# Performance work log

Hardware: AMD Instinct MI355X
Metric: run time of the kernel (lower is better)

Reference implementation:

```python
import math
import jax, jax.numpy as jnp
import numpy as np

B, N, D, H = 2, 2048, 1024, 16

def setup_inputs() -> dict:
    key = jax.random.key(0)
    ks = jax.random.split(key, 5)
    x = jax.random.normal(ks[0], (B, N, D), dtype=jnp.float32)
    # causal mask: True = masked (matches masked_fill semantics)
    mask = jnp.broadcast_to(jnp.triu(jnp.ones((N, N), dtype=bool), k=1), (B, N, N))
    sc = 0.02
    Wqkv = jax.random.normal(ks[1], (3 * D, D), dtype=jnp.float32) * sc
    bqkv = jax.random.normal(ks[2], (3 * D,), dtype=jnp.float32) * sc
    Wo = jax.random.normal(ks[3], (D, D), dtype=jnp.float32) * sc
    bo = jax.random.normal(ks[4], (D,), dtype=jnp.float32) * sc
    return {"x": x, "mask": mask, "Wqkv": Wqkv, "bqkv": bqkv, "Wo": Wo, "bo": bo}

def reference(x, mask, Wqkv, bqkv, Wo, bo):
    b, n, d = x.shape
    h = H
    s = d // h
    qkv = x @ Wqkv.T + bqkv                       # [b, n, 3d]
    q, k, v = jnp.split(qkv, 3, axis=2)           # each [b, n, d]
    def heads(z):
        return z.reshape(b, n, h, s).transpose(0, 2, 1, 3)  # [b, h, n, s]
    q, k, v = heads(q), heads(k), heads(v)
    q = q / jnp.asarray(math.sqrt(s), q.dtype)
    a = jnp.einsum('bhqs,bhks->bhqk', q, k)       # [b, h, n, n]
    a = jnp.where(mask[:, None, :, :], -jnp.inf, a)
    a = jax.nn.softmax(a, axis=-1)
    y = jnp.einsum('bhqk,bhks->bhqs', a, v)       # [b, h, n, s]
    y = y.transpose(0, 2, 1, 3).reshape(b, n, d)
    return y @ Wo.T + bo
```

## Files before the change

### kernel.cpp

```cpp
#include <hip/hip_runtime.h>
#include <hip/hip_bf16.h>
#include <stdint.h>

#define BB 2
#define NN 2048
#define DD 1024
#define HH 16
#define SS 64

typedef short short8 __attribute__((ext_vector_type(8)));
typedef float f32x4 __attribute__((ext_vector_type(4)));

__device__ __forceinline__ float bf2f(uint16_t u) {
    return __uint_as_float(((uint32_t)u) << 16);
}
__device__ __forceinline__ uint16_t f2bf(float f) {
    uint32_t u = __float_as_uint(f);
    return (uint16_t)((u + 0x7FFFu + ((u >> 16) & 1u)) >> 16);
}
__device__ __forceinline__ short8 cvt8(float4 a, float4 b) {
    short8 s;
    s[0] = (short)f2bf(a.x); s[1] = (short)f2bf(a.y);
    s[2] = (short)f2bf(a.z); s[3] = (short)f2bf(a.w);
    s[4] = (short)f2bf(b.x); s[5] = (short)f2bf(b.y);
    s[6] = (short)f2bf(b.z); s[7] = (short)f2bf(b.w);
    return s;
}

__device__ __forceinline__ void load_lds16(const uint16_t* g, uint16_t* l) {
    __builtin_amdgcn_global_load_lds(
        (const __attribute__((address_space(1))) void*)g,
        (__attribute__((address_space(3))) void*)l, 16, 0, 0);
}

#define XE  (4096 * 1024)
#define WQE (3072 * 1024)
#define WOE (1024 * 1024)

__global__ __launch_bounds__(256) void cvt_all(
    const float* __restrict__ x, const float* __restrict__ wq,
    const float* __restrict__ wo, uint16_t* __restrict__ dst)
{
    int i = (blockIdx.x * 256 + threadIdx.x) * 8;
    const float* src;
    int off;
    if (i < XE)            { src = x;  off = i; }
    else if (i < XE + WQE) { src = wq; off = i - XE; }
    else                   { src = wo; off = i - XE - WQE; }
    float4 a = *(const float4*)(src + off);
    float4 b = *(const float4*)(src + off + 4);
    *(short8*)(dst + i) = cvt8(a, b);
}

__global__ __launch_bounds__(256) void gemm_qkv(
    const uint16_t* __restrict__ X, const uint16_t* __restrict__ W,
    const float* __restrict__ bias,
    uint16_t* __restrict__ Qb, uint16_t* __restrict__ Kb, uint16_t* __restrict__ Vt)
{
    __shared__ __align__(16) uint16_t smem[18432];
    uint16_t* As0 = smem;
    uint16_t* As1 = smem + 4096;
    uint16_t* Bs0 = smem + 8192;
    uint16_t* Bs1 = smem + 12288;

    const int tid = threadIdx.x;
    const int w = tid >> 6, l = tid & 63;
    const int lq = l & 15, lg = l >> 4;
    const int wm = w >> 1, wn = w & 1;

    const int flat = blockIdx.x + blockIdx.y * 24;
    const int xcd = flat & 7, g = flat >> 3;
    const int n0 = (xcd * 3 + (g % 3)) * 128;
    const int m0 = (g / 3) * 128;

    f32x4 acc[4][4] = {};

    for (int k0 = 0; k0 < 1024; k0 += 64) {
        __syncthreads();
        #pragma unroll
        for (int j = 0; j < 2; ++j) {
            const int c = (j * 4 + w) * 64 + l;
            const size_t ra = (size_t)(m0 + (c >> 2)) * 1024 + k0 + (c & 3) * 8;
            const size_t rb = (size_t)(n0 + (c >> 2)) * 1024 + k0 + (c & 3) * 8;
            load_lds16(X + ra,      As0 + (j * 4 + w) * 512);
            load_lds16(X + ra + 32, As1 + (j * 4 + w) * 512);
            load_lds16(W + rb,      Bs0 + (j * 4 + w) * 512);
            load_lds16(W + rb + 32, Bs1 + (j * 4 + w) * 512);
        }
        __syncthreads();
        short8 af[4], bfr[4];
        #pragma unroll
        for (int mi = 0; mi < 4; ++mi)
            af[mi] = *(const short8*)&As0[(wm * 64 + mi * 16 + lq) * 32 + lg * 8];
        #pragma unroll
        for (int ni = 0; ni < 4; ++ni)
            bfr[ni] = *(const short8*)&Bs0[(wn * 64 + ni * 16 + lq) * 32 + lg * 8];
        #pragma unroll
        for (int mi = 0; mi < 4; ++mi)
            #pragma unroll
            for (int ni = 0; ni < 4; ++ni)
                acc[mi][ni] = __builtin_amdgcn_mfma_f32_16x16x32_bf16(
                    af[mi], bfr[ni], acc[mi][ni], 0, 0, 0);
        #pragma unroll
        for (int mi = 0; mi < 4; ++mi)
            af[mi] = *(const short8*)&As1[(wm * 64 + mi * 16 + lq) * 32 + lg * 8];
        #pragma unroll
        for (int ni = 0; ni < 4; ++ni)
            bfr[ni] = *(const short8*)&Bs1[(wn * 64 + ni * 16 + lq) * 32 + lg * 8];
        #pragma unroll
        for (int mi = 0; mi < 4; ++mi)
            #pragma unroll
            for (int ni = 0; ni < 4; ++ni)
                acc[mi][ni] = __builtin_amdgcn_mfma_f32_16x16x32_bf16(
                    af[mi], bfr[ni], acc[mi][ni], 0, 0, 0);
    }

    __syncthreads();
    const int part = n0 >> 10;
    const int hh = ((n0 + wn * 64) & 1023) >> 6;
    const int mrow0 = m0 + wm * 64;
    const int bh = (mrow0 >> 11) * 16 + hh;
    const int tok0 = mrow0 & 2047;
    const float scl = (part == 0) ? 0.125f * 1.44269504089f : 1.0f;

    float bias4[4];
    #pragma unroll
    for (int ni = 0; ni < 4; ++ni)
        bias4[ni] = bias[n0 + wn * 64 + ni * 16 + lq];

    uint16_t* T = smem + w * 4608;
    if (part < 2) {
        #pragma unroll
        for (int mi = 0; mi < 4; ++mi)
            #pragma unroll
            for (int ni = 0; ni < 4; ++ni)
                #pragma unroll
                for (int r = 0; r < 4; ++r)
                    T[(mi * 16 + lg * 4 + r) * 72 + ni * 16 + lq] =
                        f2bf((acc[mi][ni][r] + bias4[ni]) * scl);
    } else {
        #pragma unroll
        for (int mi = 0; mi < 4; ++mi)
            #pragma unroll
            for (int ni = 0; ni < 4; ++ni)
                #pragma unroll
                for (int r = 0; r < 4; ++r)
                    T[(ni * 16 + lq) * 72 + mi * 16 + lg * 4 + r] =
                        f2bf(acc[mi][ni][r] + bias4[ni]);
    }

    const int a0 = l >> 3, b8 = (l & 7) * 8;
    #pragma unroll
    for (int i = 0; i < 8; ++i) {
        int a = i * 8 + a0;
        short8 u = *(short8*)&T[a * 72 + b8];
        uint16_t* p;
        if (part < 2) {
            uint16_t* dst = (part == 0) ? Qb : Kb;
            p = dst + ((size_t)bh * 2048 + tok0 + a) * 64 + b8;
        } else {
            p = Vt + ((size_t)bh * 64 + a) * 2048 + tok0 + b8;
        }
        *(short8*)p = u;
    }
}

__device__ __forceinline__ void loadKf(const uint16_t* Kb, int kv0, int lq, int lg,
                                       short8 (&d)[8]) {
    #pragma unroll
    for (int n = 0; n < 4; ++n) {
        const uint16_t* kb = Kb + (size_t)(kv0 + n * 16 + lq) * 64 + lg * 8;
        d[2 * n]     = *(const short8*)kb;
        d[2 * n + 1] = *(const short8*)(kb + 32);
    }
}
__device__ __forceinline__ void loadVf(const uint16_t* Vb, int kv0, int lq, int lg,
                                       short8 (&d)[8]) {
    #pragma unroll
    for (int n = 0; n < 4; ++n) {
        const uint16_t* vb = Vb + (size_t)(n * 16 + lq) * 2048 + kv0 + lg * 8;
        d[2 * n]     = *(const short8*)vb;
        d[2 * n + 1] = *(const short8*)(vb + 32);
    }
}

#define DEFER_THR 11.5f

__global__ __launch_bounds__(128) void attn_mfma(
    const uint16_t* __restrict__ Q, const uint16_t* __restrict__ K,
    const uint16_t* __restrict__ Vt, uint16_t* __restrict__ Y)
{
    const int id = blockIdx.x;
    const int bh = id & 31;
    const int blk = 63 - (id >> 5);
    const int qt = blk >> 1;
    const int q0 = blk * 32;

    const int wv = threadIdx.x >> 6;
    const int lane = threadIdx.x & 63;
    const int lq = lane & 15;
    const int lg = lane >> 4;

    __shared__ __align__(16) uint16_t Pl[2][2][16][72];
    __shared__ float  My[32][68];
    __shared__ float2 Mml[32];

    const uint16_t* Kb = K + (size_t)bh * (2048 * 64);
    const uint16_t* Vb = Vt + (size_t)bh * (64 * 2048);
    const int b = bh >> 4, h = bh & 15;

    short8 qf[2][2];
    #pragma unroll
    for (int sub = 0; sub < 2; ++sub) {
        const uint16_t* qb = Q + ((size_t)bh * 2048 + q0 + sub * 16 + lq) * 64 + lg * 8;
        qf[sub][0] = *(const short8*)qb;
        qf[sub][1] = *(const short8*)(qb + 32);
    }

    f32x4 y[2][4] = {};
    float m[2]    = {-INFINITY, -INFINITY};
    float lsum[2] = {0.f, 0.f};

    short8 kf[8], vv[8];
    loadKf(Kb, wv * 64, lq, lg, kf);

    auto step = [&](int kv0, bool domask, bool pref) {
        loadVf(Vb, kv0, lq, lg, vv);

        f32x4 z[2][4];
        __builtin_amdgcn_s_setprio(1);
        #pragma unroll
        for (int sub = 0; sub < 2; ++sub)
            #pragma unroll
            for (int n = 0; n < 4; ++n) {
                f32x4 t = {};
                t = __builtin_amdgcn_mfma_f32_16x16x32_bf16(kf[2 * n], qf[sub][0], t, 0, 0, 0);
                z[sub][n] = __builtin_amdgcn_mfma_f32_16x16x32_bf16(kf[2 * n + 1], qf[sub][1], t, 0, 0, 0);
            }
        __builtin_amdgcn_s_setprio(0);

        if (pref) loadKf(Kb, kv0 + 128, lq, lg, kf);

        if (domask) {
            #pragma unroll
            for (int sub = 0; sub < 2; ++sub) {
                const int qrow = q0 + sub * 16 + lq;
                #pragma unroll
                for (int n = 0; n < 4; ++n) {
                    const int kvb = kv0 + n * 16 + lg * 4;
                    #pragma unroll
                    for (int r = 0; r < 4; ++r)
                        if (kvb + r > qrow) z[sub][n][r] = -INFINITY;
                }
            }
        }

        float mt[2];
        #pragma unroll
        for (int sub = 0; sub < 2; ++sub) {
            float t = -INFINITY;
            #pragma unroll
            for (int n = 0; n < 4; ++n)
                #pragma unroll
                for (int r = 0; r < 4; ++r)
                    t = fmaxf(t, z[sub][n][r]);
            mt[sub] = t;
        }
        const float g = fmaxf(mt[0] - m[0], mt[1] - m[1]);
        const bool skip = __all(g <= DEFER_THR);

        if (!skip) {
            #pragma unroll
            for (int sub = 0; sub < 2; ++sub) {
                float mf = fmaxf(mt[sub], __shfl_xor(mt[sub], 16));
                mf = fmaxf(mf, __shfl_xor(mf, 32));
                const float mn = fmaxf(m[sub], mf);
                const float sc = exp2f(m[sub] - mn);
                m[sub] = mn;
                lsum[sub] *= sc;
                float scy[4];
                #pragma unroll
                for (int r = 0; r < 4; ++r) scy[r] = __shfl(sc, lg * 4 + r);
                #pragma unroll
                for (int n = 0; n < 4; ++n)
                    #pragma unroll
                    for (int r = 0; r < 4; ++r)
                        y[sub][n][r] *= scy[r];
            }
        }

        float ps[2] = {0.f, 0.f};
        #pragma unroll
        for (int sub = 0; sub < 2; ++sub) {
            #pragma unroll
            for (int n = 0; n < 4; ++n) {
                float e0 = exp2f(z[sub][n][0] - m[sub]);
                float e1 = exp2f(z[sub][n][1] - m[sub]);
                float e2 = exp2f(z[sub][n][2] - m[sub]);
                float e3 = exp2f(z[sub][n][3] - m[sub]);
                ps[sub] += (e0 + e1) + (e2 + e3);
                uint32_t p0, p1;
                asm("v_cvt_pk_bf16_f32 %0, %1, %2" : "=v"(p0) : "v"(e0), "v"(e1));
                asm("v_cvt_pk_bf16_f32 %0, %1, %2" : "=v"(p1) : "v"(e2), "v"(e3));
                uint2 u; u.x = p0; u.y = p1;
                *(uint2*)&Pl[wv][sub][lq][n * 16 + lg * 4] = u;
            }
        }
        lsum[0] += ps[0];
        lsum[1] += ps[1];

        short8 pa[2][2];
        #pragma unroll
        for (int sub = 0; sub < 2; ++sub) {
            pa[sub][0] = *(short8*)&Pl[wv][sub][lq][lg * 8];
            pa[sub][1] = *(short8*)&Pl[wv][sub][lq][lg * 8 + 32];
        }

        __builtin_amdgcn_s_setprio(1);
        #pragma unroll
        for (int sub = 0; sub < 2; ++sub)
            #pragma unroll
            for (int n = 0; n < 4; ++n) {
                y[sub][n] = __builtin_amdgcn_mfma_f32_16x16x32_bf16(pa[sub][0], vv[2 * n], y[sub][n], 0, 0, 0);
                y[sub][n] = __builtin_amdgcn_mfma_f32_16x16x32_bf16(pa[sub][1], vv[2 * n + 1], y[sub][n], 0, 0, 0);
            }
        __builtin_amdgcn_s_setprio(0);
    };

    if (wv <= qt) {
        int kt = wv;
        for (; kt + 2 <= qt; kt += 2)
            step(kt * 64, false, true);
        step(kt * 64, kt == qt, false);
    }

    float ls[2];
    #pragma unroll
    for (int sub = 0; sub < 2; ++sub) {
        float t = lsum[sub];
        t += __shfl_xor(t, 16);
        t += __shfl_xor(t, 32);
        ls[sub] = t;
    }

    if (wv == 1) {
        #pragma unroll
        for (int sub = 0; sub < 2; ++sub) {
            #pragma unroll
            for (int n = 0; n < 4; ++n)
                #pragma unroll
                for (int r = 0; r < 4; ++r)
                    My[sub * 16 + lg * 4 + r][n * 16 + lq] = y[sub][n][r];
            if (lg == 0) Mml[sub * 16 + lq] = make_float2(m[sub], ls[sub]);
        }
    }
    __syncthreads();
    if (wv == 0) {
        #pragma unroll
        for (int sub = 0; sub < 2; ++sub) {
            float2 o = Mml[sub * 16 + lq];
            const float m1 = o.x, l1 = o.y;
            const float mx = fmaxf(m[sub], m1);
            const float w0 = exp2f(m[sub] - mx);
            const float w1 = exp2f(m1 - mx);
            const float inv = 1.0f / (ls[sub] * w0 + l1 * w1);
            const float f0 = w0 * inv, f1 = w1 * inv;
            float f0r[4], f1r[4];
            #pragma unroll
            for (int r = 0; r < 4; ++r) {
                f0r[r] = __shfl(f0, lg * 4 + r);
                f1r[r] = __shfl(f1, lg * 4 + r);
            }
            #pragma unroll
            for (int r = 0; r < 4; ++r) {
                int token = b * 2048 + q0 + sub * 16 + lg * 4 + r;
                uint16_t* yrow = Y + (size_t)token * 1024 + h * 64;
                #pragma unroll
                for (int n = 0; n < 4; ++n) {
                    float val = y[sub][n][r] * f0r[r] +
                                My[sub * 16 + lg * 4 + r][n * 16 + lq] * f1r[r];
                    yrow[n * 16 + lq] = f2bf(val);
                }
            }
        }
    }
}

__global__ __launch_bounds__(256) void gemm_proj(
    const uint16_t* __restrict__ Yin, const uint16_t* __restrict__ W,
    const float* __restrict__ bias, float* __restrict__ out)
{
    __shared__ __align__(16) uint16_t smem[16384];
    uint16_t* As0 = smem;
    uint16_t* As1 = smem + 4096;
    uint16_t* Bs0 = smem + 8192;
    uint16_t* Bs1 = smem + 12288;

    const int tid = threadIdx.x;
    const int w = tid >> 6, l = tid & 63;
    const int lq = l & 15, lg = l >> 4;
    const int wm = w >> 1, wn = w & 1;

    const int flat = blockIdx.x + blockIdx.y * 8;
    const int n0 = (flat & 7) * 128;
    const int m0 = (flat >> 3) * 128;

    f32x4 acc[4][4] = {};

    for (int k0 = 0; k0 < 1024; k0 += 64) {
        __syncthreads();
        #pragma unroll
        for (int j = 0; j < 2; ++j) {
            const int c = (j * 4 + w) * 64 + l;
            const size_t ra = (size_t)(m0 + (c >> 2)) * 1024 + k0 + (c & 3) * 8;
            const size_t rb = (size_t)(n0 + (c >> 2)) * 1024 + k0 + (c & 3) * 8;
            load_lds16(Yin + ra,      As0 + (j * 4 + w) * 512);
            load_lds16(Yin + ra + 32, As1 + (j * 4 + w) * 512);
            load_lds16(W + rb,        Bs0 + (j * 4 + w) * 512);
            load_lds16(W + rb + 32,   Bs1 + (j * 4 + w) * 512);
        }
        __syncthreads();
        short8 af[4], bfr[4];
        #pragma unroll
        for (int mi = 0; mi < 4; ++mi)
            af[mi] = *(const short8*)&As0[(wm * 64 + mi * 16 + lq) * 32 + lg * 8];
        #pragma unroll
        for (int ni = 0; ni < 4; ++ni)
            bfr[ni] = *(const short8*)&Bs0[(wn * 64 + ni * 16 + lq) * 32 + lg * 8];
        #pragma unroll
        for (int mi = 0; mi < 4; ++mi)
            #pragma unroll
            for (int ni = 0; ni < 4; ++ni)
                acc[mi][ni] = __builtin_amdgcn_mfma_f32_16x16x32_bf16(
                    af[mi], bfr[ni], acc[mi][ni], 0, 0, 0);
        #pragma unroll
        for (int mi = 0; mi < 4; ++mi)
            af[mi] = *(const short8*)&As1[(wm * 64 + mi * 16 + lq) * 32 + lg * 8];
        #pragma unroll
        for (int ni = 0; ni < 4; ++ni)
            bfr[ni] = *(const short8*)&Bs1[(wn * 64 + ni * 16 + lq) * 32 + lg * 8];
        #pragma unroll
        for (int mi = 0; mi < 4; ++mi)
            #pragma unroll
            for (int ni = 0; ni < 4; ++ni)
                acc[mi][ni] = __builtin_amdgcn_mfma_f32_16x16x32_bf16(
                    af[mi], bfr[ni], acc[mi][ni], 0, 0, 0);
    }

    const int mrow0 = m0 + wm * 64;
    const int ncol0 = n0 + wn * 64;
    float bias4[4];
    #pragma unroll
    for (int ni = 0; ni < 4; ++ni)
        bias4[ni] = bias[ncol0 + ni * 16 + lq];

    #pragma unroll
    for (int mi = 0; mi < 4; ++mi)
        #pragma unroll
        for (int r = 0; r < 4; ++r) {
            const size_t rowoff = (size_t)(mrow0 + mi * 16 + lg * 4 + r) * 1024;
            #pragma unroll
            for (int ni = 0; ni < 4; ++ni)
                out[rowoff + ncol0 + ni * 16 + lq] = acc[mi][ni][r] + bias4[ni];
        }
}


extern "C" void kernel_launch(void* const* d_in, const int* in_sizes, int n_in,
                              void* d_out, int out_size, void* d_ws, size_t ws_size,
                              hipStream_t stream) {
    const float* x    = (const float*)d_in[0];
    const float* Wqkv = (const float*)d_in[2];
    const float* bqkv = (const float*)d_in[3];
    const float* Wo   = (const float*)d_in[4];
    const float* bo   = (const float*)d_in[5];

    const size_t QK = (size_t)BB * HH * NN * SS;

    uint16_t* Xb  = (uint16_t*)d_ws;
    uint16_t* Wqb = Xb + XE;
    uint16_t* Wob = Wqb + WQE;
    uint16_t* Qb  = Wob + WOE;
    uint16_t* Kb  = Qb + QK;
    uint16_t* Vt  = Kb + QK;
    uint16_t* Yb  = Vt + QK;

    cvt_all<<<(XE + WQE + WOE) / 8 / 256, 256, 0, stream>>>(x, Wqkv, Wo, Xb);
    gemm_qkv<<<dim3(24, 32), 256, 0, stream>>>(Xb, Wqb, bqkv, Qb, Kb, Vt);
    attn_mfma<<<2048, 128, 0, stream>>>(Qb, Kb, Vt, Yb);
    gemm_proj<<<dim3(8, 32), 256, 0, stream>>>(Yb, Wob, bo, (float*)d_out);
}
```

Baseline: 139.6 us.

## Pair short and long causal query blocks per workgroup for load balance

The attention kernel now launches half as many workgroups. Each workgroup processes two query blocks, a short one (xp) and its mirrored long one (63-xp), so every workgroup does roughly the same causal work. K/V addressing also switches to precomputed per-lane pointers that advance by a fixed stride, which removes per-iteration index math. The cost is less parallelism (1024 blocks of 2 waves) and an extra __syncthreads per half, and the two halves run serially inside a block.

```diff
diff --git a/kernel.cpp b/kernel.cpp
--- a/kernel.cpp
+++ b/kernel.cpp
@@ -165,22 +165,18 @@
     }
 }
 
-__device__ __forceinline__ void loadKf(const uint16_t* Kb, int kv0, int lq, int lg,
-                                       short8 (&d)[8]) {
+__device__ __forceinline__ void loadK8(const uint16_t* kp, short8 (&d)[8]) {
     #pragma unroll
     for (int n = 0; n < 4; ++n) {
-        const uint16_t* kb = Kb + (size_t)(kv0 + n * 16 + lq) * 64 + lg * 8;
-        d[2 * n]     = *(const short8*)kb;
-        d[2 * n + 1] = *(const short8*)(kb + 32);
-    }
-}
-__device__ __forceinline__ void loadVf(const uint16_t* Vb, int kv0, int lq, int lg,
-                                       short8 (&d)[8]) {
+        d[2 * n]     = *(const short8*)(kp + n * 1024);
+        d[2 * n + 1] = *(const short8*)(kp + n * 1024 + 32);
+    }
+}
+__device__ __forceinline__ void loadV8(const uint16_t* vp, short8 (&d)[8]) {
     #pragma unroll
     for (int n = 0; n < 4; ++n) {
-        const uint16_t* vb = Vb + (size_t)(n * 16 + lq) * 2048 + kv0 + lg * 8;
-        d[2 * n]     = *(const short8*)vb;
-        d[2 * n + 1] = *(const short8*)(vb + 32);
+        d[2 * n]     = *(const short8*)(vp + n * 32768);
+        d[2 * n + 1] = *(const short8*)(vp + n * 32768 + 32);
     }
 }
 
@@ -192,9 +188,7 @@
 {
     const int id = blockIdx.x;
     const int bh = id & 31;
-    const int blk = 63 - (id >> 5);
-    const int qt = blk >> 1;
-    const int q0 = blk * 32;
+    const int xp = id >> 5;
 
     const int wv = threadIdx.x >> 6;
     const int lane = threadIdx.x & 63;
@@ -209,180 +203,194 @@
     const uint16_t* Vb = Vt + (size_t)bh * (64 * 2048);
     const int b = bh >> 4, h = bh & 15;
 
-    short8 qf[2][2];
-    #pragma unroll
-    for (int sub = 0; sub < 2; ++sub) {
-        const uint16_t* qb = Q + ((size_t)bh * 2048 + q0 + sub * 16 + lq) * 64 + lg * 8;
-        qf[sub][0] = *(const short8*)qb;
-        qf[sub][1] = *(const short8*)(qb + 32);
-    }
-
-    f32x4 y[2][4] = {};
-    float m[2]    = {-INFINITY, -INFINITY};
-    float lsum[2] = {0.f, 0.f};
-
-    short8 kf[8], vv[8];
-    loadKf(Kb, wv * 64, lq, lg, kf);
-
-    auto step = [&](int kv0, bool domask, bool pref) {
-        loadVf(Vb, kv0, lq, lg, vv);
-
-        f32x4 z[2][4];
-        __builtin_amdgcn_s_setprio(1);
-        #pragma unroll
-        for (int sub = 0; sub < 2; ++sub)
-            #pragma unroll
-            for (int n = 0; n < 4; ++n) {
-                f32x4 t = {};
-                t = __builtin_amdgcn_mfma_f32_16x16x32_bf16(kf[2 * n], qf[sub][0], t, 0, 0, 0);
-                z[sub][n] = __builtin_amdgcn_mfma_f32_16x16x32_bf16(kf[2 * n + 1], qf[sub][1], t, 0, 0, 0);
-            }
-        __builtin_amdgcn_s_setprio(0);
-
-        if (pref) loadKf(Kb, kv0 + 128, lq, lg, kf);
-
-        if (domask) {
+    for (int half = 0; half < 2; ++half) {
+        const int blk = half ? (63 - xp) : xp;
+        const int qt = blk >> 1;
+        const int q0 = blk * 32;
+
+        short8 qf[2][2];
+        #pragma unroll
+        for (int sub = 0; sub < 2; ++sub) {
+            const uint16_t* qb = Q + ((size_t)bh * 2048 + q0 + sub * 16 + lq) * 64 + lg * 8;
+            qf[sub][0] = *(const short8*)qb;
+            qf[sub][1] = *(const short8*)(qb + 32);
+        }
+
+        f32x4 y[2][4] = {};
+        float m[2]    = {-INFINITY, -INFINITY};
+        float lsum[2] = {0.f, 0.f};
+
+        const uint16_t* kp = Kb + ((size_t)(wv * 64 + lq)) * 64 + lg * 8;
+        const uint16_t* vp = Vb + (size_t)lq * 2048 + wv * 64 + lg * 8;
+
+        short8 kf[8], vv[8];
+        loadK8(kp, kf);
+
+        auto step = [&](int kv0, const uint16_t* vcur, const uint16_t* knext,
+                        bool domask, bool pref) {
+            loadV8(vcur, vv);
+
+            f32x4 z[2][4];
+            __builtin_amdgcn_s_setprio(1);
+            #pragma unroll
+            for (int sub = 0; sub < 2; ++sub)
+                #pragma unroll
+                for (int n = 0; n < 4; ++n) {
+                    f32x4 t = {};
+                    t = __builtin_amdgcn_mfma_f32_16x16x32_bf16(kf[2 * n], qf[sub][0], t, 0, 0, 0);
+                    z[sub][n] = __builtin_amdgcn_mfma_f32_16x16x32_bf16(kf[2 * n + 1], qf[sub][1], t, 0, 0, 0);
+                }
+            __builtin_amdgcn_s_setprio(0);
+
+            if (pref) loadK8(knext, kf);
+
+            if (domask) {
+                #pragma unroll
+                for (int sub = 0; sub < 2; ++sub) {
+                    const int qrow = q0 + sub * 16 + lq;
+                    #pragma unroll
+                    for (int n = 0; n < 4; ++n) {
+                        const int kvb = kv0 + n * 16 + lg * 4;
+                        #pragma unroll
+                        for (int r = 0; r < 4; ++r)
+                            if (kvb + r > qrow) z[sub][n][r] = -INFINITY;
+                    }
+                }
+            }
+
+            float mt[2];
             #pragma unroll
             for (int sub = 0; sub < 2; ++sub) {
-                const int qrow = q0 + sub * 16 + lq;
-                #pragma unroll
-                for (int n = 0; n < 4; ++n) {
-                    const int kvb = kv0 + n * 16 + lg * 4;
-                    #pragma unroll
-                    for (int r = 0; r < 4; ++r)
-                        if (kvb + r > qrow) z[sub][n][r] = -INFINITY;
-                }
-            }
-        }
-
-        float mt[2];
-        #pragma unroll
-        for (int sub = 0; sub < 2; ++sub) {
-            float t = -INFINITY;
-            #pragma unroll
-            for (int n = 0; n < 4; ++n)
-                #pragma unroll
-                for (int r = 0; r < 4; ++r)
-                    t = fmaxf(t, z[sub][n][r]);
-            mt[sub] = t;
-        }
-        const float g = fmaxf(mt[0] - m[0], mt[1] - m[1]);
-        const bool skip = __all(g <= DEFER_THR);
-
-        if (!skip) {
-            #pragma unroll
-            for (int sub = 0; sub < 2; ++sub) {
-                float mf = fmaxf(mt[sub], __shfl_xor(mt[sub], 16));
-                mf = fmaxf(mf, __shfl_xor(mf, 32));
-                const float mn = fmaxf(m[sub], mf);
-                const float sc = exp2f(m[sub] - mn);
-                m[sub] = mn;
-                lsum[sub] *= sc;
-                float scy[4];
-                #pragma unroll
-                for (int r = 0; r < 4; ++r) scy[r] = __shfl(sc, lg * 4 + r);
+                float t = -INFINITY;
                 #pragma unroll
                 for (int n = 0; n < 4; ++n)
                     #pragma unroll
                     for (int r = 0; r < 4; ++r)
-                        y[sub][n][r] *= scy[r];
-            }
-        }
-
-        float ps[2] = {0.f, 0.f};
+                        t = fmaxf(t, z[sub][n][r]);
+                mt[sub] = t;
+            }
+            const float g = fmaxf(mt[0] - m[0], mt[1] - m[1]);
+            const bool skip = __all(g <= DEFER_THR);
+
+            if (!skip) {
+                #pragma unroll
+                for (int sub = 0; sub < 2; ++sub) {
+                    float mf = fmaxf(mt[sub], __shfl_xor(mt[sub], 16));
+                    mf = fmaxf(mf, __shfl_xor(mf, 32));
+                    const float mn = fmaxf(m[sub], mf);
+                    const float sc = exp2f(m[sub] - mn);
+                    m[sub] = mn;
+                    lsum[sub] *= sc;
+                    float scy[4];
+                    #pragma unroll
+                    for (int r = 0; r < 4; ++r) scy[r] = __shfl(sc, lg * 4 + r);
+                    #pragma unroll
+                    for (int n = 0; n < 4; ++n)
+                        #pragma unroll
+                        for (int r = 0; r < 4; ++r)
+                            y[sub][n][r] *= scy[r];
+                }
+            }
+
+            float ps[2] = {0.f, 0.f};
+            #pragma unroll
+            for (int sub = 0; sub < 2; ++sub) {
+                #pragma unroll
+                for (int n = 0; n < 4; ++n) {
+                    float e0 = exp2f(z[sub][n][0] - m[sub]);
+                    float e1 = exp2f(z[sub][n][1] - m[sub]);
+                    float e2 = exp2f(z[sub][n][2] - m[sub]);
+                    float e3 = exp2f(z[sub][n][3] - m[sub]);
+                    ps[sub] += (e0 + e1) + (e2 + e3);
+                    uint32_t p0, p1;
+                    asm("v_cvt_pk_bf16_f32 %0, %1, %2" : "=v"(p0) : "v"(e0), "v"(e1));
+                    asm("v_cvt_pk_bf16_f32 %0, %1, %2" : "=v"(p1) : "v"(e2), "v"(e3));
+                    uint2 u; u.x = p0; u.y = p1;
+                    *(uint2*)&Pl[wv][sub][lq][n * 16 + lg * 4] = u;
+                }
+            }
+            lsum[0] += ps[0];
+            lsum[1] += ps[1];
+
+            short8 pa[2][2];
+            #pragma unroll
+            for (int sub = 0; sub < 2; ++sub) {
+                pa[sub][0] = *(short8*)&Pl[wv][sub][lq][lg * 8];
+                pa[sub][1] = *(short8*)&Pl[wv][sub][lq][lg * 8 + 32];
+            }
+
+            __builtin_amdgcn_s_setprio(1);
+            #pragma unroll
+            for (int sub = 0; sub < 2; ++sub)
+                #pragma unroll
+                for (int n = 0; n < 4; ++n) {
+                    y[sub][n] = __builtin_amdgcn_mfma_f32_16x16x32_bf16(pa[sub][0], vv[2 * n], y[sub][n], 0, 0, 0);
+                    y[sub][n] = __builtin_amdgcn_mfma_f32_16x16x32_bf16(pa[sub][1], vv[2 * n + 1], y[sub][n], 0, 0, 0);
+                }
+            __builtin_amdgcn_s_setprio(0);
+        };
+
+        if (wv <= qt) {
+            int kt = wv;
+            for (; kt + 2 <= qt; kt += 2) {
+                step(kt * 64, vp, kp + 8192, false, true);
+                kp += 8192;
+                vp += 128;
+            }
+            step(kt * 64, vp, kp, kt == qt, false);
+        }
+
+        float ls[2];
         #pragma unroll
         for (int sub = 0; sub < 2; ++sub) {
-            #pragma unroll
-            for (int n = 0; n < 4; ++n) {
-                float e0 = exp2f(z[sub][n][0] - m[sub]);
-                float e1 = exp2f(z[sub][n][1] - m[sub]);
-                float e2 = exp2f(z[sub][n][2] - m[sub]);
-                float e3 = exp2f(z[sub][n][3] - m[sub]);
-                ps[sub] += (e0 + e1) + (e2 + e3);
-                uint32_t p0, p1;
-                asm("v_cvt_pk_bf16_f32 %0, %1, %2" : "=v"(p0) : "v"(e0), "v"(e1));
-                asm("v_cvt_pk_bf16_f32 %0, %1, %2" : "=v"(p1) : "v"(e2), "v"(e3));
-                uint2 u; u.x = p0; u.y = p1;
-                *(uint2*)&Pl[wv][sub][lq][n * 16 + lg * 4] = u;
-            }
-        }
-        lsum[0] += ps[0];
-        lsum[1] += ps[1];
-
-        short8 pa[2][2];
-        #pragma unroll
-        for (int sub = 0; sub < 2; ++sub) {
-            pa[sub][0] = *(short8*)&Pl[wv][sub][lq][lg * 8];
-            pa[sub][1] = *(short8*)&Pl[wv][sub][lq][lg * 8 + 32];
-        }
-
-        __builtin_amdgcn_s_setprio(1);
-        #pragma unroll
-        for (int sub = 0; sub < 2; ++sub)
-            #pragma unroll
-            for (int n = 0; n < 4; ++n) {
-                y[sub][n] = __builtin_amdgcn_mfma_f32_16x16x32_bf16(pa[sub][0], vv[2 * n], y[sub][n], 0, 0, 0);
-                y[sub][n] = __builtin_amdgcn_mfma_f32_16x16x32_bf16(pa[sub][1], vv[2 * n + 1], y[sub][n], 0, 0, 0);
-            }
-        __builtin_amdgcn_s_setprio(0);
-    };
-
-    if (wv <= qt) {
-        int kt = wv;
-        for (; kt + 2 <= qt; kt += 2)
-            step(kt * 64, false, true);
-        step(kt * 64, kt == qt, false);
-    }
-
-    float ls[2];
-    #pragma unroll
-    for (int sub = 0; sub < 2; ++sub) {
-        float t = lsum[sub];
-        t += __shfl_xor(t, 16);
-        t += __shfl_xor(t, 32);
-        ls[sub] = t;
-    }
-
-    if (wv == 1) {
-        #pragma unroll
-        for (int sub = 0; sub < 2; ++sub) {
-            #pragma unroll
-            for (int n = 0; n < 4; ++n)
-                #pragma unroll
-                for (int r = 0; r < 4; ++r)
-                    My[sub * 16 + lg * 4 + r][n * 16 + lq] = y[sub][n][r];
-            if (lg == 0) Mml[sub * 16 + lq] = make_float2(m[sub], ls[sub]);
-        }
-    }
-    __syncthreads();
-    if (wv == 0) {
-        #pragma unroll
-        for (int sub = 0; sub < 2; ++sub) {
-            float2 o = Mml[sub * 16 + lq];
-            const float m1 = o.x, l1 = o.y;
-            const float mx = fmaxf(m[sub], m1);
-            const float w0 = exp2f(m[sub] - mx);
-            const float w1 = exp2f(m1 - mx);
-            const float inv = 1.0f / (ls[sub] * w0 + l1 * w1);
-            const float f0 = w0 * inv, f1 = w1 * inv;
-            float f0r[4], f1r[4];
-            #pragma unroll
-            for (int r = 0; r < 4; ++r) {
-                f0r[r] = __shfl(f0, lg * 4 + r);
-                f1r[r] = __shfl(f1, lg * 4 + r);
-            }
-            #pragma unroll
-            for (int r = 0; r < 4; ++r) {
-                int token = b * 2048 + q0 + sub * 16 + lg * 4 + r;
-                uint16_t* yrow = Y + (size_t)token * 1024 + h * 64;
-                #pragma unroll
-                for (int n = 0; n < 4; ++n) {
-                    float val = y[sub][n][r] * f0r[r] +
-                                My[sub * 16 + lg * 4 + r][n * 16 + lq] * f1r[r];
-                    yrow[n * 16 + lq] = f2bf(val);
-                }
-            }
-        }
+            float t = lsum[sub];
+            t += __shfl_xor(t, 16);
+            t += __shfl_xor(t, 32);
+            ls[sub] = t;
+        }
+
+        if (wv == 1) {
+            #pragma unroll
+            for (int sub = 0; sub < 2; ++sub) {
+                #pragma unroll
+                for (int n = 0; n < 4; ++n)
+                    #pragma unroll
+                    for (int r = 0; r < 4; ++r)
+                        My[sub * 16 + lg * 4 + r][n * 16 + lq] = y[sub][n][r];
+                if (lg == 0) Mml[sub * 16 + lq] = make_float2(m[sub], ls[sub]);
+            }
+        }
+        __syncthreads();
+        if (wv == 0) {
+            #pragma unroll
+            for (int sub = 0; sub < 2; ++sub) {
+                float2 o = Mml[sub * 16 + lq];
+                const float m1 = o.x, l1 = o.y;
+                const float mx = fmaxf(m[sub], m1);
+                const float w0 = exp2f(m[sub] - mx);
+                const float w1 = exp2f(m1 - mx);
+                const float inv = 1.0f / (ls[sub] * w0 + l1 * w1);
+                const float f0 = w0 * inv, f1 = w1 * inv;
+                float f0r[4], f1r[4];
+                #pragma unroll
+                for (int r = 0; r < 4; ++r) {
+                    f0r[r] = __shfl(f0, lg * 4 + r);
+                    f1r[r] = __shfl(f1, lg * 4 + r);
+                }
+                #pragma unroll
+                for (int r = 0; r < 4; ++r) {
+                    int token = b * 2048 + q0 + sub * 16 + lg * 4 + r;
+                    uint16_t* yrow = Y + (size_t)token * 1024 + h * 64;
+                    #pragma unroll
+                    for (int n = 0; n < 4; ++n) {
+                        float val = y[sub][n][r] * f0r[r] +
+                                    My[sub * 16 + lg * 4 + r][n * 16 + lq] * f1r[r];
+                        yrow[n * 16 + lq] = f2bf(val);
+                    }
+                }
+            }
+        }
+        __syncthreads();
     }
 }
 
@@ -487,6 +495,6 @@
 
     cvt_all<<<(XE + WQE + WOE) / 8 / 256, 256, 0, stream>>>(x, Wqkv, Wo, Xb);
     gemm_qkv<<<dim3(24, 32), 256, 0, stream>>>(Xb, Wqb, bqkv, Qb, Kb, Vt);
-    attn_mfma<<<2048, 128, 0, stream>>>(Qb, Kb, Vt, Yb);
+    attn_mfma<<<1024, 128, 0, stream>>>(Qb, Kb, Vt, Yb);
     gemm_proj<<<dim3(8, 32), 256, 0, stream>>>(Yb, Wob, bo, (float*)d_out);
 }
```

Measured after the change: 140.7 us. About the same (+0.8%).
